# Kernel tuning notes

Measured on AMD Instinct MI355X. Metric: run time of the kernel, lower is better.

## Reference

```python
import jax, jax.numpy as jnp
import numpy as np

NEG_SLOPE = 0.2
EPS = 1e-16
HEADS1, OUT1 = 4, 32
HEADS2, OUT2 = 1, 32


def _gat_conv(x, W, a_src, a_dst, bias, src, dst, num_nodes, heads, out_c, concat):
    # x: [N, F_in], W: [F_in, heads*out_c], a_*: [heads, out_c]
    h = (x @ W).reshape(num_nodes, heads, out_c)            # [N, H, C]
    alpha_src = (h * a_src).sum(-1)                          # [N, H]
    alpha_dst = (h * a_dst).sum(-1)                          # [N, H]
    e = jax.nn.leaky_relu(alpha_src[src] + alpha_dst[dst], NEG_SLOPE)  # [E, H]
    # softmax over incoming edges of each destination node (PyG softmax)
    m = jax.ops.segment_max(e, dst, num_segments=num_nodes)
    ex = jnp.exp(e - m[dst])
    s = jax.ops.segment_sum(ex, dst, num_segments=num_nodes)
    alpha = ex / (s[dst] + EPS)                              # [E, H]
    out = jax.ops.segment_sum(h[src] * alpha[:, :, None], dst,
                              num_segments=num_nodes)        # [N, H, C]
    out = out.reshape(num_nodes, heads * out_c) if concat else out.mean(axis=1)
    return out + bias


def setup_inputs() -> dict:
    key = jax.random.key(0)
    ks = jax.random.split(key, 10)
    N, E, F_IN = 50000, 1600000, 128
    sc = 0.1
    return {
        "x": jax.random.normal(ks[0], (N, F_IN), jnp.float32),
        "edge_index": jax.random.randint(ks[1], (2, E), 0, N, jnp.int32),
        "W1": jax.random.normal(ks[2], (F_IN, HEADS1 * OUT1), jnp.float32) * sc,
        "a_src1": jax.random.normal(ks[3], (HEADS1, OUT1), jnp.float32) * sc,
        "a_dst1": jax.random.normal(ks[4], (HEADS1, OUT1), jnp.float32) * sc,
        "b1": jax.random.normal(ks[5], (HEADS1 * OUT1,), jnp.float32) * sc,
        "W2": jax.random.normal(ks[6], (HEADS1 * OUT1, HEADS2 * OUT2), jnp.float32) * sc,
        "a_src2": jax.random.normal(ks[7], (HEADS2, OUT2), jnp.float32) * sc,
        "a_dst2": jax.random.normal(ks[8], (HEADS2, OUT2), jnp.float32) * sc,
        "b2": jax.random.normal(ks[9], (OUT2,), jnp.float32) * sc,
    }


def reference(x, edge_index, W1, a_src1, a_dst1, b1, W2, a_src2, a_dst2, b2):
    N = x.shape[0]
    # PyG GATConv default add_self_loops=True
    loops = jnp.arange(N, dtype=edge_index.dtype)
    src = jnp.concatenate([edge_index[0], loops])
    dst = jnp.concatenate([edge_index[1], loops])
    h = _gat_conv(x, W1, a_src1, a_dst1, b1, src, dst, N, HEADS1, OUT1, True)
    h = jax.nn.elu(h)
    return _gat_conv(h, W2, a_src2, a_dst2, b2, src, dst, N, HEADS2, OUT2, False)
```

## Files before the change

### kernel.cpp

```cpp
#include <hip/hip_runtime.h>
#include <math.h>

#define NEG_SLOPE 0.2f
#define EPSV 1e-16f
#define NPART 4

typedef _Float16 half4 __attribute__((ext_vector_type(4)));
typedef _Float16 half8 __attribute__((ext_vector_type(8)));
typedef float floatx2 __attribute__((ext_vector_type(2)));


__global__ void k_scan_blk(const int* __restrict__ degp, int N,
                           int* __restrict__ rowptr, int* __restrict__ bsum){
    int b = blockIdx.x, t = threadIdx.x;
    int base = b * 1024 + t * 4;
    int v[4];
    #pragma unroll
    for (int j = 0; j < 4; j++){
        int n = base + j, s = 0;
        if (n < N){
            #pragma unroll
            for (int p = 0; p < NPART; p++) s += degp[p * N + n];
        }
        v[j] = s;
    }
    int s = v[0] + v[1] + v[2] + v[3];
    int lane = t & 63, wid = t >> 6;
    int x = s;
    #pragma unroll
    for (int off = 1; off < 64; off <<= 1){
        int y = __shfl_up(x, off, 64);
        if (lane >= off) x += y;
    }
    __shared__ int ws[4];
    if (lane == 63) ws[wid] = x;
    __syncthreads();
    int woff = 0;
    for (int w = 0; w < wid; w++) woff += ws[w];
    int run = woff + x - s;
    #pragma unroll
    for (int j = 0; j < 4; j++){
        if (base + j < N) rowptr[base + j] = run;
        run += v[j];
    }
    if (t == 255) bsum[b] = woff + x;
}

__global__ void k_finalize(const int* __restrict__ bsum, const int* __restrict__ degp,
                           int N, int ET,
                           int* __restrict__ rowptr, int* __restrict__ poff){
    int b = blockIdx.x, t = threadIdx.x;
    int n = b * 256 + t;
    int chunk = (b * 256) >> 10;
    int off = 0;
    for (int c = 0; c < chunk; c++) off += bsum[c];
    if (n < N){
        int r = rowptr[n] + off;
        rowptr[n] = r;
        int run = r;
        #pragma unroll
        for (int p = 0; p < NPART; p++){
            poff[p * N + n] = run;
            run += degp[p * N + n];
        }
    }
    if (n == 0) rowptr[N] = ET;
}

__launch_bounds__(256)
__global__ void k_scatter2(const int* __restrict__ ei, int E, int ET, int N,
                           const int* __restrict__ poff,
                           const unsigned short* __restrict__ rank,
                           int* __restrict__ csr_src){
    int i = blockIdx.x * 256 + threadIdx.x;
    if (i >= ET) return;
    int s, d;
    if (i < E){ s = ei[i]; d = ei[E + i]; } else { s = i - E; d = s; }
    int p = (i >> 8) & (NPART - 1);
    csr_src[poff[p * N + d] + (int)rank[i]] = s;
}


__launch_bounds__(256)
__global__ void k_gemm1_hist(const float* __restrict__ x, const float* __restrict__ W1,
                             const float* __restrict__ a_src, const float* __restrict__ a_dst,
                             _Float16* __restrict__ h1h, float* __restrict__ asrc1,
                             float* __restrict__ adst1, int N, int nGemmBlk,
                             const int* __restrict__ ei, int E, int ET,
                             int* __restrict__ degp, unsigned short* __restrict__ rank){
    __shared__ float Wl[16 * 128];
    __shared__ float xl[32 * 128];
    int t = threadIdx.x;
    if ((int)blockIdx.x >= nGemmBlk){
        int base = (blockIdx.x - nGemmBlk) * 1024 + t;
        #pragma unroll
        for (int j = 0; j < 4; j++){
            int i = base + j * 256;
            if (i < ET){
                int d = (i < E) ? ei[E + i] : (i - E);
                int p = (i >> 8) & (NPART - 1);
                rank[i] = (unsigned short)atomicAdd(&degp[p * N + d], 1);
            }
        }
        return;
    }
    int cg = t & 31, ns = t >> 5;
    int n0 = blockIdx.x * 32;
    for (int idx = t; idx < 1024; idx += 256){
        int row = idx >> 5, k4 = idx & 31;
        float4 v = {0.f, 0.f, 0.f, 0.f};
        if (n0 + row < N) v = *(const float4*)&x[(size_t)(n0 + row) * 128 + k4 * 4];
        *(float4*)&xl[row * 128 + k4 * 4] = v;
    }
    float4 acc0 = {0,0,0,0}, acc1 = {0,0,0,0}, acc2 = {0,0,0,0}, acc3 = {0,0,0,0};
    for (int c = 0; c < 8; c++){
        __syncthreads();
        for (int idx = t; idx < 512; idx += 256)
            *(float4*)&Wl[idx * 4] = *(const float4*)&W1[c * 16 * 128 + idx * 4];
        __syncthreads();
        #pragma unroll
        for (int k = 0; k < 16; k += 4){
            float4 xv0 = *(float4*)&xl[(ns     ) * 128 + c * 16 + k];
            float4 xv1 = *(float4*)&xl[(ns +  8) * 128 + c * 16 + k];
            float4 xv2 = *(float4*)&xl[(ns + 16) * 128 + c * 16 + k];
            float4 xv3 = *(float4*)&xl[(ns + 24) * 128 + c * 16 + k];
            #pragma unroll
            for (int kk = 0; kk < 4; kk++){
                float4 w = *(float4*)&Wl[(k + kk) * 128 + cg * 4];
                float x0 = ((float*)&xv0)[kk];
                float x1 = ((float*)&xv1)[kk];
                float x2v= ((float*)&xv2)[kk];
                float x3 = ((float*)&xv3)[kk];
                acc0.x = fmaf(x0, w.x, acc0.x); acc0.y = fmaf(x0, w.y, acc0.y);
                acc0.z = fmaf(x0, w.z, acc0.z); acc0.w = fmaf(x0, w.w, acc0.w);
                acc1.x = fmaf(x1, w.x, acc1.x); acc1.y = fmaf(x1, w.y, acc1.y);
                acc1.z = fmaf(x1, w.z, acc1.z); acc1.w = fmaf(x1, w.w, acc1.w);
                acc2.x = fmaf(x2v, w.x, acc2.x); acc2.y = fmaf(x2v, w.y, acc2.y);
                acc2.z = fmaf(x2v, w.z, acc2.z); acc2.w = fmaf(x2v, w.w, acc2.w);
                acc3.x = fmaf(x3, w.x, acc3.x); acc3.y = fmaf(x3, w.y, acc3.y);
                acc3.z = fmaf(x3, w.z, acc3.z); acc3.w = fmaf(x3, w.w, acc3.w);
            }
        }
    }
    float4 a4s = *(const float4*)&a_src[cg * 4];
    float4 a4d = *(const float4*)&a_dst[cg * 4];
    float4 accs[4] = {acc0, acc1, acc2, acc3};
    #pragma unroll
    for (int j = 0; j < 4; j++){
        int n = n0 + ns + 8 * j;
        if (n >= N) continue;
        float4 a = accs[j];
        half4 hv;
        hv.x = (_Float16)a.x; hv.y = (_Float16)a.y;
        hv.z = (_Float16)a.z; hv.w = (_Float16)a.w;
        *(half4*)&h1h[((size_t)n << 7) + (cg << 2)] = hv;
        float vs = a.x * a4s.x + a.y * a4s.y + a.z * a4s.z + a.w * a4s.w;
        float vd = a.x * a4d.x + a.y * a4d.y + a.z * a4d.z + a.w * a4d.w;
        #pragma unroll
        for (int m = 1; m <= 4; m <<= 1){
            vs += __shfl_xor(vs, m, 64);
            vd += __shfl_xor(vd, m, 64);
        }
        if ((cg & 7) == 0){
            int head = cg >> 3;
            asrc1[n * 4 + head] = vs;
            adst1[n * 4 + head] = vd;
        }
    }
}


__launch_bounds__(256)
__global__ void k_agg1(const int* __restrict__ rowptr, const int* __restrict__ csr_src,
                       const float* __restrict__ asrc1, const float* __restrict__ adst1,
                       const _Float16* __restrict__ h1h,
                       const float* __restrict__ b1, float* __restrict__ x2){
    int t = threadIdx.x;
    int n = blockIdx.x * 4 + (t >> 6);
    int lane = t & 63, g = lane >> 4, l = lane & 15, head = l >> 2;
    int start = rowptr[n], end = rowptr[n + 1];
    float adn = adst1[(n << 2) + head];
    const char* hb = (const char*)h1h;
    const char* ab = (const char*)asrc1;
    int hoff = l << 4;
    int aoff = head << 2;
    floatx2 rA[4], rB[4];
    #pragma unroll
    for (int j = 0; j < 4; j++){ rA[j] = (floatx2)0.f; rB[j] = (floatx2)0.f; }
    float sA = 0.f, sB = 0.f;
    int i = start + g;
    for (; i + 4 < end; i += 8){
        int s0 = csr_src[i];
        int s1 = csr_src[i + 4];
        float e0 = *(const float*)(ab + (s0 << 4) + aoff) + adn;
        float e1 = *(const float*)(ab + (s1 << 4) + aoff) + adn;
        e0 = fmaxf(e0, NEG_SLOPE * e0);
        e1 = fmaxf(e1, NEG_SLOPE * e1);
        float w0 = __expf(e0);
        float w1 = __expf(e1);
        half8 h0 = *(const half8*)(hb + (s0 << 8) + hoff);
        half8 h1v = *(const half8*)(hb + (s1 << 8) + hoff);
        sA += w0; sB += w1;
        floatx2 w02 = {w0, w0}, w12 = {w1, w1};
        #pragma unroll
        for (int j = 0; j < 4; j++){
            floatx2 c0 = {(float)h0[2*j], (float)h0[2*j+1]};
            floatx2 c1 = {(float)h1v[2*j], (float)h1v[2*j+1]};
            rA[j] = w02 * c0 + rA[j];
            rB[j] = w12 * c1 + rB[j];
        }
    }
    if (i < end){
        int s0 = csr_src[i];
        float e0 = *(const float*)(ab + (s0 << 4) + aoff) + adn;
        e0 = fmaxf(e0, NEG_SLOPE * e0);
        float w0 = __expf(e0);
        half8 h0 = *(const half8*)(hb + (s0 << 8) + hoff);
        sA += w0;
        floatx2 w02 = {w0, w0};
        #pragma unroll
        for (int j = 0; j < 4; j++){
            floatx2 c0 = {(float)h0[2*j], (float)h0[2*j+1]};
            rA[j] = w02 * c0 + rA[j];
        }
    }
    float r[9];
    #pragma unroll
    for (int j = 0; j < 4; j++){
        floatx2 c = rA[j] + rB[j];
        r[2*j] = c.x; r[2*j+1] = c.y;
    }
    r[8] = sA + sB;
    #pragma unroll
    for (int m = 16; m <= 32; m <<= 1)
        #pragma unroll
        for (int j = 0; j < 9; j++) r[j] += __shfl_xor(r[j], m, 64);
    if (g == 0){
        float inv = 1.f / (r[8] + EPSV);
        float o[8];
        #pragma unroll
        for (int j = 0; j < 8; j++){
            float v = r[j] * inv + b1[l * 8 + j];
            o[j] = (v > 0.f) ? v : expm1f(v);
        }
        float4 o0 = {o[0], o[1], o[2], o[3]};
        float4 o1 = {o[4], o[5], o[6], o[7]};
        *(float4*)&x2[((size_t)n << 7) + (l << 3)]     = o0;
        *(float4*)&x2[((size_t)n << 7) + (l << 3) + 4] = o1;
    }
}


__launch_bounds__(256)
__global__ void k_gemm2(const float* __restrict__ x2, const float* __restrict__ W2,
                        const float* __restrict__ a_src, const float* __restrict__ a_dst,
                        _Float16* __restrict__ h2h, float* __restrict__ asrc2,
                        float* __restrict__ adst2, int N){
    __shared__ float Wl[128 * 32];
    __shared__ float xl[64 * 128];
    int t = threadIdx.x;
    int cg = t & 7, ns = t >> 3;
    for (int idx = t; idx < 1024; idx += 256)
        *(float4*)&Wl[idx * 4] = *(const float4*)&W2[idx * 4];
    int n0 = blockIdx.x * 64;
    for (int idx = t; idx < 2048; idx += 256){
        int row = idx >> 5, k4 = idx & 31;
        float4 v = {0.f, 0.f, 0.f, 0.f};
        if (n0 + row < N) v = *(const float4*)&x2[(size_t)(n0 + row) * 128 + k4 * 4];
        *(float4*)&xl[row * 128 + k4 * 4] = v;
    }
    __syncthreads();
    float4 acc0 = {0,0,0,0}, acc1 = {0,0,0,0};
    #pragma unroll 2
    for (int k = 0; k < 128; k += 4){
        float4 xv0 = *(float4*)&xl[(ns      ) * 128 + k];
        float4 xv1 = *(float4*)&xl[(ns + 32) * 128 + k];
        #pragma unroll
        for (int kk = 0; kk < 4; kk++){
            float4 w = *(float4*)&Wl[(k + kk) * 32 + cg * 4];
            float x0 = ((float*)&xv0)[kk];
            float x1 = ((float*)&xv1)[kk];
            acc0.x = fmaf(x0, w.x, acc0.x); acc0.y = fmaf(x0, w.y, acc0.y);
            acc0.z = fmaf(x0, w.z, acc0.z); acc0.w = fmaf(x0, w.w, acc0.w);
            acc1.x = fmaf(x1, w.x, acc1.x); acc1.y = fmaf(x1, w.y, acc1.y);
            acc1.z = fmaf(x1, w.z, acc1.z); acc1.w = fmaf(x1, w.w, acc1.w);
        }
    }
    float4 a4s = *(const float4*)&a_src[cg * 4];
    float4 a4d = *(const float4*)&a_dst[cg * 4];
    float4 accs[2] = {acc0, acc1};
    #pragma unroll
    for (int j = 0; j < 2; j++){
        int n = n0 + ns + 32 * j;
        if (n >= N) continue;
        float4 a = accs[j];
        half4 hv;
        hv.x = (_Float16)a.x; hv.y = (_Float16)a.y;
        hv.z = (_Float16)a.z; hv.w = (_Float16)a.w;
        *(half4*)&h2h[((size_t)n << 5) + (cg << 2)] = hv;
        float vs = a.x * a4s.x + a.y * a4s.y + a.z * a4s.z + a.w * a4s.w;
        float vd = a.x * a4d.x + a.y * a4d.y + a.z * a4d.z + a.w * a4d.w;
        #pragma unroll
        for (int m = 1; m <= 4; m <<= 1){
            vs += __shfl_xor(vs, m, 64);
            vd += __shfl_xor(vd, m, 64);
        }
        if (cg == 0){ asrc2[n] = vs; adst2[n] = vd; }
    }
}


__launch_bounds__(256)
__global__ void k_agg2(const int* __restrict__ rowptr, const int* __restrict__ csr_src,
                       const float* __restrict__ asrc2, const float* __restrict__ adst2,
                       const _Float16* __restrict__ h2h,
                       const float* __restrict__ b2, float* __restrict__ out){
    int t = threadIdx.x;
    int n = blockIdx.x * 8 + (t >> 5);
    int l5 = t & 31, g = l5 >> 3, l = l5 & 7;
    int start = rowptr[n], end = rowptr[n + 1];
    float adn = adst2[n];
    const char* hb = (const char*)h2h;
    const char* ab = (const char*)asrc2;
    int hoff = l << 3;
    floatx2 aA[2], aB[2];
    aA[0] = (floatx2)0.f; aA[1] = (floatx2)0.f;
    aB[0] = (floatx2)0.f; aB[1] = (floatx2)0.f;
    float sA = 0.f, sB = 0.f;
    int i = start + g;
    for (; i + 4 < end; i += 8){
        int s0 = csr_src[i];
        int s1 = csr_src[i + 4];
        float e0 = *(const float*)(ab + (s0 << 2)) + adn;
        float e1 = *(const float*)(ab + (s1 << 2)) + adn;
        e0 = fmaxf(e0, NEG_SLOPE * e0);
        e1 = fmaxf(e1, NEG_SLOPE * e1);
        float w0 = __expf(e0);
        float w1 = __expf(e1);
        half4 h0 = *(const half4*)(hb + (s0 << 6) + hoff);
        half4 h1v = *(const half4*)(hb + (s1 << 6) + hoff);
        sA += w0; sB += w1;
        floatx2 w02 = {w0, w0}, w12 = {w1, w1};
        floatx2 c00 = {(float)h0.x, (float)h0.y}, c01 = {(float)h0.z, (float)h0.w};
        floatx2 c10 = {(float)h1v.x, (float)h1v.y}, c11 = {(float)h1v.z, (float)h1v.w};
        aA[0] = w02 * c00 + aA[0]; aA[1] = w02 * c01 + aA[1];
        aB[0] = w12 * c10 + aB[0]; aB[1] = w12 * c11 + aB[1];
    }
    if (i < end){
        int s0 = csr_src[i];
        float e0 = *(const float*)(ab + (s0 << 2)) + adn;
        e0 = fmaxf(e0, NEG_SLOPE * e0);
        float w0 = __expf(e0);
        half4 h0 = *(const half4*)(hb + (s0 << 6) + hoff);
        sA += w0;
        floatx2 w02 = {w0, w0};
        floatx2 c00 = {(float)h0.x, (float)h0.y}, c01 = {(float)h0.z, (float)h0.w};
        aA[0] = w02 * c00 + aA[0]; aA[1] = w02 * c01 + aA[1];
    }
    floatx2 m0 = aA[0] + aB[0], m1 = aA[1] + aB[1];
    float4 acc = {m0.x, m0.y, m1.x, m1.y};
    float ssum = sA + sB;
    #pragma unroll
    for (int m = 8; m <= 16; m <<= 1){
        acc.x += __shfl_xor(acc.x, m, 64);
        acc.y += __shfl_xor(acc.y, m, 64);
        acc.z += __shfl_xor(acc.z, m, 64);
        acc.w += __shfl_xor(acc.w, m, 64);
        ssum  += __shfl_xor(ssum,  m, 64);
    }
    if (g == 0){
        float inv = 1.f / (ssum + EPSV);
        const float4 b4 = *(const float4*)&b2[l * 4];
        float4 o;
        o.x = acc.x * inv + b4.x; o.y = acc.y * inv + b4.y;
        o.z = acc.z * inv + b4.z; o.w = acc.w * inv + b4.w;
        *(float4*)&out[((size_t)n << 5) + l * 4] = o;
    }
}


extern "C" void kernel_launch(void* const* d_in, const int* in_sizes, int n_in,
                              void* d_out, int out_size, void* d_ws, size_t ws_size,
                              hipStream_t stream){
    const float* x      = (const float*)d_in[0];
    const int*   ei     = (const int*)  d_in[1];
    const float* W1     = (const float*)d_in[2];
    const float* a_src1 = (const float*)d_in[3];
    const float* a_dst1 = (const float*)d_in[4];
    const float* b1     = (const float*)d_in[5];
    const float* W2     = (const float*)d_in[6];
    const float* a_src2 = (const float*)d_in[7];
    const float* a_dst2 = (const float*)d_in[8];
    const float* b2     = (const float*)d_in[9];
    float* out = (float*)d_out;

    int N  = in_sizes[0] / 128;
    int E  = in_sizes[1] / 2;
    int ET = E + N;
    int nScanBlk = (N + 1023) / 1024;
    int G  = (ET + 255) / 256;
    int GH = (ET + 1023) / 1024;
    int nGemmBlk = (N + 31) / 32;

    char* ws = (char*)d_ws;
    size_t off = 0;
    auto alloc = [&](size_t bytes) -> char* {
        char* p = ws + off;
        off += (bytes + 255) & ~(size_t)255;
        return p;
    };
    int*            degp    = (int*)           alloc((size_t)NPART * N * 4);
    int*            rowptr  = (int*)           alloc((size_t)(N + 1) * 4);
    int*            bsum    = (int*)           alloc((size_t)nScanBlk * 4);
    unsigned short* rank    = (unsigned short*)alloc((size_t)ET * 2);
    int*            poff    = (int*)           alloc((size_t)NPART * N * 4);
    int*            csr_src = (int*)           alloc((size_t)ET * 4);
    _Float16*       h1h     = (_Float16*)      alloc((size_t)N * 128 * 2);
    float*          x2      = (float*)         alloc((size_t)N * 128 * 4);
    float*          asrc1   = (float*)         alloc((size_t)N * 4 * 4);
    float*          adst1   = (float*)         alloc((size_t)N * 4 * 4);
    _Float16*       h2h     = (_Float16*)      alloc((size_t)N * 32 * 2);
    float*          asrc2   = (float*)         alloc((size_t)N * 4);
    float*          adst2   = (float*)         alloc((size_t)N * 4);

    hipMemsetAsync(degp, 0, (size_t)NPART * N * 4, stream);
    hipLaunchKernelGGL(k_gemm1_hist, dim3(nGemmBlk + GH), dim3(256), 0, stream,
                       x, W1, a_src1, a_dst1, h1h, asrc1, adst1, N, nGemmBlk,
                       ei, E, ET, degp, rank);
    hipLaunchKernelGGL(k_scan_blk,  dim3(nScanBlk), dim3(256), 0, stream, degp, N, rowptr, bsum);
    hipLaunchKernelGGL(k_finalize,  dim3((N + 255) / 256), dim3(256), 0, stream, bsum, degp, N, ET, rowptr, poff);
    hipLaunchKernelGGL(k_scatter2,  dim3(G), dim3(256), 0, stream, ei, E, ET, N, poff, rank, csr_src);
    hipLaunchKernelGGL(k_agg1,      dim3(N / 4), dim3(256), 0, stream, rowptr, csr_src, asrc1, adst1, h1h, b1, x2);
    hipLaunchKernelGGL(k_gemm2,     dim3((N + 63) / 64), dim3(256), 0, stream, x2, W2, a_src2, a_dst2, h2h, asrc2, adst2, N);
    hipLaunchKernelGGL(k_agg2,      dim3(N / 8), dim3(256), 0, stream, rowptr, csr_src, asrc2, adst2, h2h, b2, out);
}
```

Baseline: 305.1 us.

## Replace global atomic degree histogram with per-chunk LDS packed 16-bit histograms

```diff
diff --git a/kernel.cpp b/kernel.cpp
--- a/kernel.cpp
+++ b/kernel.cpp
@@ -3,27 +3,72 @@
 
 #define NEG_SLOPE 0.2f
 #define EPSV 1e-16f
-#define NPART 4
+#define NCHUNK 256
+#define LDSW 25088
 
 typedef _Float16 half4 __attribute__((ext_vector_type(4)));
 typedef _Float16 half8 __attribute__((ext_vector_type(8)));
 typedef float floatx2 __attribute__((ext_vector_type(2)));
 
 
-__global__ void k_scan_blk(const int* __restrict__ degp, int N,
+__launch_bounds__(256)
+__global__ void k_p1(const int* __restrict__ ei, int E, int ET, int N, int ipc,
+                     unsigned short* __restrict__ rank, unsigned short* __restrict__ cnt16){
+    __shared__ unsigned int cnt[LDSW];
+    int t = threadIdx.x, b = blockIdx.x;
+    int words = (N + 1) >> 1;
+    for (int idx = t; idx < words; idx += 256) cnt[idx] = 0;
+    __syncthreads();
+    int chunkSz = ipc << 8;
+    int base = b * chunkSz + t;
+    for (int it0 = 0; it0 < ipc; it0 += 8){
+        int dv[8];
+        #pragma unroll
+        for (int j = 0; j < 8; j++){
+            int it = it0 + j;
+            int i = base + (it << 8);
+            int d = -1;
+            if (it < ipc && i < ET) d = (i < E) ? ei[E + i] : (i - E);
+            dv[j] = d;
+        }
+        #pragma unroll
+        for (int j = 0; j < 8; j++){
+            int d = dv[j];
+            if (d >= 0){
+                int i = base + ((it0 + j) << 8);
+                unsigned int sh = (unsigned int)(d & 1) << 4;
+                unsigned int old = atomicAdd(&cnt[d >> 1], 1u << sh);
+                rank[i] = (unsigned short)((old >> sh) & 0xffffu);
+            }
+        }
+    }
+    __syncthreads();
+    unsigned int* row = (unsigned int*)(cnt16 + (size_t)b * (unsigned)((N + 1) & ~1));
+    for (int idx = t; idx < words; idx += 256) row[idx] = cnt[idx];
+}
+
+__global__ void k_combine(unsigned short* __restrict__ cnt16, int N, int* __restrict__ deg){
+    int d = blockIdx.x * 256 + threadIdx.x;
+    if (d >= N) return;
+    size_t NW = (size_t)((N + 1) & ~1);
+    unsigned short* p = cnt16 + d;
+    int run = 0;
+    #pragma unroll 8
+    for (int b = 0; b < NCHUNK; b++){
+        int c = p[(size_t)b * NW];
+        p[(size_t)b * NW] = (unsigned short)run;
+        run += c;
+    }
+    deg[d] = run;
+}
+
+__global__ void k_scan_blk(const int* __restrict__ deg, int N,
                            int* __restrict__ rowptr, int* __restrict__ bsum){
     int b = blockIdx.x, t = threadIdx.x;
     int base = b * 1024 + t * 4;
     int v[4];
     #pragma unroll
-    for (int j = 0; j < 4; j++){
-        int n = base + j, s = 0;
-        if (n < N){
-            #pragma unroll
-            for (int p = 0; p < NPART; p++) s += degp[p * N + n];
-        }
-        v[j] = s;
-    }
+    for (int j = 0; j < 4; j++) v[j] = (base + j < N) ? deg[base + j] : 0;
     int s = v[0] + v[1] + v[2] + v[3];
     int lane = t & 63, wid = t >> 6;
     int x = s;
@@ -46,64 +91,42 @@
     if (t == 255) bsum[b] = woff + x;
 }
 
-__global__ void k_finalize(const int* __restrict__ bsum, const int* __restrict__ degp,
-                           int N, int ET,
-                           int* __restrict__ rowptr, int* __restrict__ poff){
+__global__ void k_finalize(const int* __restrict__ bsum, int N, int ET,
+                           int* __restrict__ rowptr){
     int b = blockIdx.x, t = threadIdx.x;
     int n = b * 256 + t;
     int chunk = (b * 256) >> 10;
     int off = 0;
     for (int c = 0; c < chunk; c++) off += bsum[c];
-    if (n < N){
-        int r = rowptr[n] + off;
-        rowptr[n] = r;
-        int run = r;
-        #pragma unroll
-        for (int p = 0; p < NPART; p++){
-            poff[p * N + n] = run;
-            run += degp[p * N + n];
-        }
-    }
+    if (n < N) rowptr[n] += off;
     if (n == 0) rowptr[N] = ET;
 }
 
 __launch_bounds__(256)
-__global__ void k_scatter2(const int* __restrict__ ei, int E, int ET, int N,
-                           const int* __restrict__ poff,
-                           const unsigned short* __restrict__ rank,
-                           int* __restrict__ csr_src){
+__global__ void k_scatter(const int* __restrict__ ei, int E, int ET, int N, int ipc,
+                          const int* __restrict__ rowptr,
+                          const unsigned short* __restrict__ cnt16,
+                          const unsigned short* __restrict__ rank,
+                          int* __restrict__ csr_src){
     int i = blockIdx.x * 256 + threadIdx.x;
     if (i >= ET) return;
     int s, d;
     if (i < E){ s = ei[i]; d = ei[E + i]; } else { s = i - E; d = s; }
-    int p = (i >> 8) & (NPART - 1);
-    csr_src[poff[p * N + d] + (int)rank[i]] = s;
-}
-
-
-__launch_bounds__(256)
-__global__ void k_gemm1_hist(const float* __restrict__ x, const float* __restrict__ W1,
-                             const float* __restrict__ a_src, const float* __restrict__ a_dst,
-                             _Float16* __restrict__ h1h, float* __restrict__ asrc1,
-                             float* __restrict__ adst1, int N, int nGemmBlk,
-                             const int* __restrict__ ei, int E, int ET,
-                             int* __restrict__ degp, unsigned short* __restrict__ rank){
+    int b = (int)blockIdx.x / ipc;
+    size_t NW = (size_t)((N + 1) & ~1);
+    int pos = rowptr[d] + (int)cnt16[(size_t)b * NW + d] + (int)rank[i];
+    csr_src[pos] = s;
+}
+
+
+__launch_bounds__(256)
+__global__ void k_gemm1(const float* __restrict__ x, const float* __restrict__ W1,
+                        const float* __restrict__ a_src, const float* __restrict__ a_dst,
+                        _Float16* __restrict__ h1h, float* __restrict__ asrc1,
+                        float* __restrict__ adst1, int N){
     __shared__ float Wl[16 * 128];
     __shared__ float xl[32 * 128];
     int t = threadIdx.x;
-    if ((int)blockIdx.x >= nGemmBlk){
-        int base = (blockIdx.x - nGemmBlk) * 1024 + t;
-        #pragma unroll
-        for (int j = 0; j < 4; j++){
-            int i = base + j * 256;
-            if (i < ET){
-                int d = (i < E) ? ei[E + i] : (i - E);
-                int p = (i >> 8) & (NPART - 1);
-                rank[i] = (unsigned short)atomicAdd(&degp[p * N + d], 1);
-            }
-        }
-        return;
-    }
     int cg = t & 31, ns = t >> 5;
     int n0 = blockIdx.x * 32;
     for (int idx = t; idx < 1024; idx += 256){
@@ -399,8 +422,8 @@
     int ET = E + N;
     int nScanBlk = (N + 1023) / 1024;
     int G  = (ET + 255) / 256;
-    int GH = (ET + 1023) / 1024;
-    int nGemmBlk = (N + 31) / 32;
+    int ipc = (ET + NCHUNK * 256 - 1) / (NCHUNK * 256);
+    int NW = (N + 1) & ~1;
 
     char* ws = (char*)d_ws;
     size_t off = 0;
@@ -409,11 +432,11 @@
         off += (bytes + 255) & ~(size_t)255;
         return p;
     };
-    int*            degp    = (int*)           alloc((size_t)NPART * N * 4);
+    unsigned short* cnt16   = (unsigned short*)alloc((size_t)NCHUNK * NW * 2);
+    unsigned short* rank    = (unsigned short*)alloc((size_t)ET * 2);
+    int*            deg     = (int*)           alloc((size_t)N * 4);
     int*            rowptr  = (int*)           alloc((size_t)(N + 1) * 4);
     int*            bsum    = (int*)           alloc((size_t)nScanBlk * 4);
-    unsigned short* rank    = (unsigned short*)alloc((size_t)ET * 2);
-    int*            poff    = (int*)           alloc((size_t)NPART * N * 4);
     int*            csr_src = (int*)           alloc((size_t)ET * 4);
     _Float16*       h1h     = (_Float16*)      alloc((size_t)N * 128 * 2);
     float*          x2      = (float*)         alloc((size_t)N * 128 * 4);
@@ -423,14 +446,13 @@
     float*          asrc2   = (float*)         alloc((size_t)N * 4);
     float*          adst2   = (float*)         alloc((size_t)N * 4);
 
-    hipMemsetAsync(degp, 0, (size_t)NPART * N * 4, stream);
-    hipLaunchKernelGGL(k_gemm1_hist, dim3(nGemmBlk + GH), dim3(256), 0, stream,
-                       x, W1, a_src1, a_dst1, h1h, asrc1, adst1, N, nGemmBlk,
-                       ei, E, ET, degp, rank);
-    hipLaunchKernelGGL(k_scan_blk,  dim3(nScanBlk), dim3(256), 0, stream, degp, N, rowptr, bsum);
-    hipLaunchKernelGGL(k_finalize,  dim3((N + 255) / 256), dim3(256), 0, stream, bsum, degp, N, ET, rowptr, poff);
-    hipLaunchKernelGGL(k_scatter2,  dim3(G), dim3(256), 0, stream, ei, E, ET, N, poff, rank, csr_src);
-    hipLaunchKernelGGL(k_agg1,      dim3(N / 4), dim3(256), 0, stream, rowptr, csr_src, asrc1, adst1, h1h, b1, x2);
-    hipLaunchKernelGGL(k_gemm2,     dim3((N + 63) / 64), dim3(256), 0, stream, x2, W2, a_src2, a_dst2, h2h, asrc2, adst2, N);
-    hipLaunchKernelGGL(k_agg2,      dim3(N / 8), dim3(256), 0, stream, rowptr, csr_src, asrc2, adst2, h2h, b2, out);
-}
+    hipLaunchKernelGGL(k_p1,       dim3(NCHUNK), dim3(256), 0, stream, ei, E, ET, N, ipc, rank, cnt16);
+    hipLaunchKernelGGL(k_gemm1,    dim3((N + 31) / 32), dim3(256), 0, stream, x, W1, a_src1, a_dst1, h1h, asrc1, adst1, N);
+    hipLaunchKernelGGL(k_combine,  dim3((N + 255) / 256), dim3(256), 0, stream, cnt16, N, deg);
+    hipLaunchKernelGGL(k_scan_blk, dim3(nScanBlk), dim3(256), 0, stream, deg, N, rowptr, bsum);
+    hipLaunchKernelGGL(k_finalize, dim3((N + 255) / 256), dim3(256), 0, stream, bsum, N, ET, rowptr);
+    hipLaunchKernelGGL(k_scatter,  dim3(G), dim3(256), 0, stream, ei, E, ET, N, ipc, rowptr, cnt16, rank, csr_src);
+    hipLaunchKernelGGL(k_agg1,     dim3(N / 4), dim3(256), 0, stream, rowptr, csr_src, asrc1, adst1, h1h, b1, x2);
+    hipLaunchKernelGGL(k_gemm2,    dim3((N + 63) / 64), dim3(256), 0, stream, x2, W2, a_src2, a_dst2, h2h, asrc2, adst2, N);
+    hipLaunchKernelGGL(k_agg2,     dim3(N / 8), dim3(256), 0, stream, rowptr, csr_src, asrc2, adst2, h2h, b2, out);
+}
```

New measurement: 322.6 us. +5.7%, slower.
